# Performance work log

Hardware: AMD Instinct MI355X
Metric: run time of the kernel (lower is better)

Reference implementation:

```python
import jax, jax.numpy as jnp
import numpy as np

N, E, L, HEADS, HID = 50000, 600000, 4, 8, 128
IN_C, OUT_C = 64, 64
D_HEAD = HID // HEADS


def _layer_norm(x, g, b, eps=1e-5):
    m = jnp.mean(x, axis=-1, keepdims=True)
    v = jnp.mean((x - m) ** 2, axis=-1, keepdims=True)
    return (x - m) * jax.lax.rsqrt(v + eps) * g + b


def _transformer_conv(h, src, dst, Wq, bq, Wk, bk, Wv, bv, Ws, bs, Wbeta):
    # PyG TransformerConv with beta=True, concat=True. src=edge_index[0] (j), dst=edge_index[1] (i).
    n, f = h.shape
    q = (h @ Wq.T + bq)[dst].reshape(-1, HEADS, D_HEAD)   # [E,H,D] query at destination
    k = (h @ Wk.T + bk)[src].reshape(-1, HEADS, D_HEAD)   # [E,H,D] key at source
    v = (h @ Wv.T + bv)[src].reshape(-1, HEADS, D_HEAD)   # [E,H,D] value at source
    alpha = jnp.sum(q * k, axis=-1) / float(np.sqrt(D_HEAD))  # [E,H]
    amax = jax.ops.segment_max(alpha, dst, num_segments=n)     # [N,H] segment softmax (stable)
    ex = jnp.exp(alpha - amax[dst])
    denom = jax.ops.segment_sum(ex, dst, num_segments=n)
    a = ex / (denom[dst] + 1e-16)                              # [E,H]
    out = jax.ops.segment_sum((a[:, :, None] * v).reshape(-1, f), dst, num_segments=n)  # [N,F]
    x_r = h @ Ws.T + bs                                        # root/skip transform
    beta = jax.nn.sigmoid(jnp.concatenate([out, x_r, out - x_r], axis=-1) @ Wbeta.T)    # [N,1]
    return beta * x_r + (1.0 - beta) * out


def _forward(x, src, dst, Wi, bi, Wq, bq, Wk, bk, Wv, bv, Ws, bs, Wbeta, ln_g, ln_b, W1, b1, W2, b2, Wo, bo):
    h = jax.nn.gelu(x @ Wi.T + bi, approximate=False)
    for i in range(L):
        res = h
        h = _transformer_conv(h, src, dst, Wq[i], bq[i], Wk[i], bk[i], Wv[i], bv[i], Ws[i], bs[i], Wbeta[i])
        h = _layer_norm(h + res, ln_g[i], ln_b[i])
        res = h
        f = jax.nn.gelu(h @ W1[i].T + b1[i], approximate=False) @ W2[i].T + b2[i]
        h = f + res
    return h @ Wo.T + bo


def setup_inputs() -> dict:
    key = jax.random.key(0)
    ks = jax.random.split(key, 24)
    rn = lambda k, shp, s=0.05: (jax.random.normal(k, shp, jnp.float32) * s)
    x = jax.random.normal(ks[0], (N, IN_C), jnp.float32)
    edge_index = jax.random.randint(ks[1], (2, E), 0, N, dtype=jnp.int64)
    return {
        "x": x,
        "edge_index": edge_index,
        "Wi": rn(ks[2], (HID, IN_C)), "bi": jnp.zeros((HID,), jnp.float32),
        "Wq": rn(ks[3], (L, HID, HID)), "bq": jnp.zeros((L, HID), jnp.float32),
        "Wk": rn(ks[4], (L, HID, HID)), "bk": jnp.zeros((L, HID), jnp.float32),
        "Wv": rn(ks[5], (L, HID, HID)), "bv": jnp.zeros((L, HID), jnp.float32),
        "Ws": rn(ks[6], (L, HID, HID)), "bs": jnp.zeros((L, HID), jnp.float32),
        "Wbeta": rn(ks[7], (L, 1, 3 * HID)),
        "ln_g": jnp.ones((L, HID), jnp.float32), "ln_b": jnp.zeros((L, HID), jnp.float32),
        "W1": rn(ks[8], (L, 4 * HID, HID)), "b1": jnp.zeros((L, 4 * HID), jnp.float32),
        "W2": rn(ks[9], (L, HID, 4 * HID)), "b2": jnp.zeros((L, HID), jnp.float32),
        "Wo": rn(ks[10], (OUT_C, HID)), "bo": jnp.zeros((OUT_C,), jnp.float32),
    }


def reference(x, edge_index, Wi, bi, Wq, bq, Wk, bk, Wv, bv, Ws, bs, Wbeta, ln_g, ln_b, W1, b1, W2, b2, Wo, bo):
    src, dst = edge_index[0], edge_index[1]
    return _forward(x, src, dst, Wi, bi, Wq, bq, Wk, bk, Wv, bv, Ws, bs, Wbeta, ln_g, ln_b, W1, b1, W2, b2, Wo, bo)
```

## Files before the change

### kernel.cpp

```cpp
#include <hip/hip_runtime.h>
#include <cmath>

#define HIDC   128
#define LAYERS 4
#define IN_C   64
#define OUT_C  64

typedef _Float16 h16x8 __attribute__((ext_vector_type(8)));
typedef _Float16 h16x2 __attribute__((ext_vector_type(2)));
typedef float    f32x4 __attribute__((ext_vector_type(4)));

__device__ __forceinline__ float gelu_f(float x) {
    return 0.5f * x * (1.0f + erff(x * 0.70710678118654752f));
}

__device__ __forceinline__ void cvt8(const float4& a, const float4& b, h16x8& h) {
    h[0]=(_Float16)a.x; h[1]=(_Float16)a.y; h[2]=(_Float16)a.z; h[3]=(_Float16)a.w;
    h[4]=(_Float16)b.x; h[5]=(_Float16)b.y; h[6]=(_Float16)b.z; h[7]=(_Float16)b.w;
}
__device__ __forceinline__ void load16(const float* p, _Float16* d) {
    float4 v0 = *(const float4*)p,     v1 = *(const float4*)(p + 4);
    float4 v2 = *(const float4*)(p+8), v3 = *(const float4*)(p + 12);
    h16x8 h0, h1; cvt8(v0, v1, h0); cvt8(v2, v3, h1);
    *(h16x8*)d = h0; *(h16x8*)(d + 8) = h1;
}
__device__ __forceinline__ void load16(const _Float16* p, _Float16* d) {
    *(h16x8*)d = *(const h16x8*)p; *(h16x8*)(d + 8) = *(const h16x8*)(p + 8);
}
__device__ __forceinline__ void zero16(_Float16* d) {
    h16x8 z = {};
    *(h16x8*)d = z; *(h16x8*)(d + 8) = z;
}

__global__ void count_deg_k(const int* __restrict__ dst, int* __restrict__ cnt, int E) {
    int i = blockIdx.x * blockDim.x + threadIdx.x;
    if (i < E) atomicAdd(&cnt[dst[i]], 1);
}

__global__ __launch_bounds__(1024)
void scan_k(const int* __restrict__ cnt, int* __restrict__ rowptr, int n) {
    __shared__ int partials[1024];
    int tid = threadIdx.x;
    int per = (n + 1023) / 1024;
    int start = tid * per;
    int end = start + per; if (end > n) end = n;
    int s = 0;
    for (int i = start; i < end; ++i) s += cnt[i];
    partials[tid] = s;
    __syncthreads();
    for (int off = 1; off < 1024; off <<= 1) {
        int v = (tid >= off) ? partials[tid - off] : 0;
        __syncthreads();
        partials[tid] += v;
        __syncthreads();
    }
    int run = (tid == 0) ? 0 : partials[tid - 1];
    for (int i = start; i < end; ++i) { rowptr[i] = run; run += cnt[i]; }
    if (tid == 1023) rowptr[n] = partials[1023];
}

__global__ void scatter_k(const int* __restrict__ src, const int* __restrict__ dst,
                          const int* __restrict__ rowptr, int* __restrict__ cnt,
                          int* __restrict__ csrc, int E) {
    int i = blockIdx.x * blockDim.x + threadIdx.x;
    if (i < E) {
        int d = dst[i];
        int pos = rowptr[d] + atomicAdd(&cnt[d], 1);
        csrc[pos] = src[i];
    }
}

template<int ACT, bool RES, bool NGUARD, typename AT, typename CT>
__device__ __forceinline__ void gemm_core(
    const AT* __restrict__ A, const float* __restrict__ Wt,
    const float* __restrict__ bias, const float* __restrict__ resid,
    CT* __restrict__ Ct, int M, int K, int ncs, int colbase, int nclim)
{
    __shared__ __align__(16) _Float16 As[128 * 40];
    __shared__ __align__(16) _Float16 Bs[128 * 40];
    const int tid  = threadIdx.x;
    const int lane = tid & 63;
    const int wave = tid >> 6;
    const int wr = wave >> 1, wc = wave & 1;
    const int row0 = blockIdx.y * 128;

    f32x4 acc[4][4] = {};

    const int srow = tid >> 1;
    const int skc  = (tid & 1) * 16;
    const int fr   = lane & 15;
    const int fk   = (lane >> 4) * 8;

    for (int k0 = 0; k0 < K; k0 += 32) {
        {
            int gr = row0 + srow;
            _Float16* d = As + srow * 40 + skc;
            if (gr < M) load16(A + (size_t)gr * K + k0 + skc, d);
            else        zero16(d);
        }
        {
            int gc = colbase + srow;
            _Float16* d = Bs + srow * 40 + skc;
            if (!NGUARD || gc < nclim) load16(Wt + (size_t)gc * K + k0 + skc, d);
            else                       zero16(d);
        }
        __syncthreads();
        h16x8 af[4], bf[4];
#pragma unroll
        for (int mi = 0; mi < 4; ++mi)
            af[mi] = *(const h16x8*)(As + (wr * 64 + mi * 16 + fr) * 40 + fk);
#pragma unroll
        for (int ni = 0; ni < 4; ++ni)
            bf[ni] = *(const h16x8*)(Bs + (wc * 64 + ni * 16 + fr) * 40 + fk);
#pragma unroll
        for (int mi = 0; mi < 4; ++mi)
#pragma unroll
            for (int ni = 0; ni < 4; ++ni)
                acc[mi][ni] = __builtin_amdgcn_mfma_f32_16x16x32_f16(af[mi], bf[ni], acc[mi][ni], 0, 0, 0);
        __syncthreads();
    }

    const int rbase = row0 + wr * 64 + ((lane >> 4) * 4);
    const int cbase = colbase + wc * 64 + fr;
#pragma unroll
    for (int mi = 0; mi < 4; ++mi) {
#pragma unroll
        for (int j = 0; j < 4; ++j) {
            int r = rbase + mi * 16 + j;
            if (r >= M) continue;
            size_t rb = (size_t)r * ncs;
#pragma unroll
            for (int ni = 0; ni < 4; ++ni) {
                int c = cbase + ni * 16;
                if (NGUARD && c >= nclim) continue;
                float v = acc[mi][ni][j] + bias[c];
                if (ACT == 1) v = gelu_f(v);
                if (RES) v += resid[rb + c];
                Ct[rb + c] = (CT)v;
            }
        }
    }
}

template<int ACT, bool RES, bool NGUARD, typename AT, typename CT>
__global__ __launch_bounds__(256)
void gemm_f16_k(const AT* __restrict__ A, const float* __restrict__ W,
                const float* __restrict__ bias, const float* __restrict__ resid,
                CT* __restrict__ C, int M, int NC, int K) {
    gemm_core<ACT, RES, NGUARD, AT, CT>(A, W, bias, resid, C, M, K, NC, blockIdx.x * 128, NC);
}

__global__ __launch_bounds__(256)
void qkvs_k(const float* __restrict__ A,
            const float* __restrict__ Wq, const float* __restrict__ Wk,
            const float* __restrict__ Wv, const float* __restrict__ Wvs,
            const float* __restrict__ bq, const float* __restrict__ bk,
            const float* __restrict__ bv, const float* __restrict__ bs,
            _Float16* __restrict__ qh, _Float16* __restrict__ kv,
            float* __restrict__ sb, int M) {
    __shared__ __align__(16) _Float16 As[128 * 136];
    __shared__ __align__(16) _Float16 Bs[128 * 136];
    const int tid  = threadIdx.x;
    const int lane = tid & 63;
    const int wave = tid >> 6;
    const int wr = wave >> 1, wc = wave & 1;
    const int row0 = blockIdx.x * 128;
    const int srow  = tid >> 1;
    const int shalf = (tid & 1) * 64;
    const int fr = lane & 15;

    {
        int gr = row0 + srow;
        _Float16* d = As + srow * 136 + shalf;
        if (gr < M) {
            const float* p = A + (size_t)gr * 128 + shalf;
#pragma unroll
            for (int u = 0; u < 4; ++u) load16(p + u * 16, d + u * 16);
        } else {
#pragma unroll
            for (int u = 0; u < 4; ++u) zero16(d + u * 16);
        }
    }

    for (int w = 0; w < 4; ++w) {
        const float* Wp = (w == 0) ? Wq : (w == 1) ? Wk : (w == 2) ? Wv : Wvs;
        const float* bp = (w == 0) ? bq : (w == 1) ? bk : (w == 2) ? bv : bs;
        {
            const float* p = Wp + (size_t)srow * 128 + shalf;
            _Float16* d = Bs + srow * 136 + shalf;
#pragma unroll
            for (int u = 0; u < 4; ++u) load16(p + u * 16, d + u * 16);
        }
        __syncthreads();
        f32x4 acc[4][4] = {};
#pragma unroll
        for (int ks = 0; ks < 4; ++ks) {
            const int fk = ks * 32 + (lane >> 4) * 8;
            h16x8 af[4], bf[4];
#pragma unroll
            for (int mi = 0; mi < 4; ++mi)
                af[mi] = *(const h16x8*)(As + (wr * 64 + mi * 16 + fr) * 136 + fk);
#pragma unroll
            for (int ni = 0; ni < 4; ++ni)
                bf[ni] = *(const h16x8*)(Bs + (wc * 64 + ni * 16 + fr) * 136 + fk);
#pragma unroll
            for (int mi = 0; mi < 4; ++mi)
#pragma unroll
                for (int ni = 0; ni < 4; ++ni)
                    acc[mi][ni] = __builtin_amdgcn_mfma_f32_16x16x32_f16(af[mi], bf[ni], acc[mi][ni], 0, 0, 0);
        }
        __syncthreads();

        const int rbase = row0 + wr * 64 + ((lane >> 4) * 4);
        const int cbase = wc * 64 + fr;
#pragma unroll
        for (int mi = 0; mi < 4; ++mi) {
#pragma unroll
            for (int j = 0; j < 4; ++j) {
                int r = rbase + mi * 16 + j;
                if (r >= M) continue;
#pragma unroll
                for (int ni = 0; ni < 4; ++ni) {
                    int c = cbase + ni * 16;
                    float v = acc[mi][ni][j] + bp[c];
                    if (w == 0)      qh[(size_t)r * 128 + c] = (_Float16)v;
                    else if (w == 1) kv[(size_t)r * 256 + c] = (_Float16)v;
                    else if (w == 2) kv[(size_t)r * 256 + 128 + c] = (_Float16)v;
                    else             sb[(size_t)r * 128 + c] = v;
                }
            }
        }
    }
}

__global__ __launch_bounds__(256)
void attn_ln_k(const _Float16* __restrict__ qh, const _Float16* __restrict__ kv,
               const int* __restrict__ rowptr, const int* __restrict__ csrc,
               const float* __restrict__ xr, const float* __restrict__ res,
               const float* __restrict__ Wb, const float* __restrict__ g_,
               const float* __restrict__ b_, float* __restrict__ out, int n) {
    int node = (int)((blockIdx.x * (size_t)blockDim.x + threadIdx.x) >> 6);
    int lane = threadIdx.x & 63;
    if (node >= n) return;
    const int g = lane & 7;
    const int h = lane >> 3;

    const _Float16* qp = qh + (size_t)node * 128 + h * 16;
    h16x8 q0 = *(const h16x8*)(qp);
    h16x8 q1 = *(const h16x8*)(qp + 8);

    float ssum = 0.f;
    float acc[16] = {};
    const int e0 = rowptr[node], e1 = rowptr[node + 1];
    for (int eb = e0; eb < e1; eb += 8) {
        int e = eb + g;
        bool val = (e < e1);
        int s = csrc[val ? e : (e1 - 1)];
        const _Float16* kp = kv + (size_t)s * 256 + h * 16;
        h16x8 k0 = *(const h16x8*)(kp);
        h16x8 k1 = *(const h16x8*)(kp + 8);
        h16x8 v0 = *(const h16x8*)(kp + 128);
        h16x8 v1 = *(const h16x8*)(kp + 136);
        float d = 0.f;
#pragma unroll
        for (int j = 0; j < 8; ++j) d += (float)k0[j] * (float)q0[j];
#pragma unroll
        for (int j = 0; j < 8; ++j) d += (float)k1[j] * (float)q1[j];
        float w = val ? __expf(d * 0.25f) : 0.f;
        ssum += w;
#pragma unroll
        for (int j = 0; j < 8; ++j) acc[j]     += w * (float)v0[j];
#pragma unroll
        for (int j = 0; j < 8; ++j) acc[8 + j] += w * (float)v1[j];
    }
#pragma unroll
    for (int m = 1; m < 8; m <<= 1) {
        ssum += __shfl_xor(ssum, m);
#pragma unroll
        for (int j = 0; j < 16; ++j) acc[j] += __shfl_xor(acc[j], m);
    }
    float inv = 1.f / (ssum + 1e-16f);
    const bool s0b = g & 1, s1b = g & 2, s2b = g & 4;
    float t0 = s0b ? acc[2]  : acc[0],  t1 = s0b ? acc[6]  : acc[4];
    float t2 = s0b ? acc[10] : acc[8],  t3 = s0b ? acc[14] : acc[12];
    float u0 = s1b ? t1 : t0,           u1 = s1b ? t3 : t2;
    float ox = (s2b ? u1 : u0) * inv;
    float p0 = s0b ? acc[3]  : acc[1],  p1 = s0b ? acc[7]  : acc[5];
    float p2 = s0b ? acc[11] : acc[9],  p3 = s0b ? acc[15] : acc[13];
    float w0 = s1b ? p1 : p0,           w1 = s1b ? p3 : p2;
    float oy = (s2b ? w1 : w0) * inv;

    size_t base = (size_t)node * HIDC + lane * 2;
    int c = lane * 2;
    float2 r  = *(const float2*)(xr + base);
    float2 wb0 = *(const float2*)(Wb + c);
    float2 wb1 = *(const float2*)(Wb + HIDC + c);
    float2 wb2 = *(const float2*)(Wb + 2 * HIDC + c);
    float part = ox * wb0.x + oy * wb0.y
               + r.x * wb1.x + r.y * wb1.y
               + (ox - r.x) * wb2.x + (oy - r.y) * wb2.y;
#pragma unroll
    for (int mk = 1; mk < 64; mk <<= 1) part += __shfl_xor(part, mk);
    float beta = 1.f / (1.f + __expf(-part));
    float2 rs = *(const float2*)(res + base);
    float tx = beta * r.x + (1.f - beta) * ox + rs.x;
    float ty = beta * r.y + (1.f - beta) * oy + rs.y;
    float sum = tx + ty;
#pragma unroll
    for (int mk = 1; mk < 64; mk <<= 1) sum += __shfl_xor(sum, mk);
    float mean = sum * (1.f / 128.f);
    float dx = tx - mean, dy = ty - mean;
    float vs = dx * dx + dy * dy;
#pragma unroll
    for (int mk = 1; mk < 64; mk <<= 1) vs += __shfl_xor(vs, mk);
    float rstd = 1.f / sqrtf(vs * (1.f / 128.f) + 1e-5f);
    float2 gg = *(const float2*)(g_ + c);
    float2 bb = *(const float2*)(b_ + c);
    float2 oo = make_float2(dx * rstd * gg.x + bb.x, dy * rstd * gg.y + bb.y);
    *(float2*)(out + base) = oo;
}

extern "C" void kernel_launch(void* const* d_in, const int* in_sizes, int n_in,
                              void* d_out, int out_size, void* d_ws, size_t ws_size,
                              hipStream_t stream) {
    const float* x    = (const float*)d_in[0];
    const int*   ei   = (const int*)d_in[1];
    const float* Wi   = (const float*)d_in[2];
    const float* bi   = (const float*)d_in[3];
    const float* Wq   = (const float*)d_in[4];
    const float* bq   = (const float*)d_in[5];
    const float* Wk   = (const float*)d_in[6];
    const float* bk   = (const float*)d_in[7];
    const float* Wv   = (const float*)d_in[8];
    const float* bv   = (const float*)d_in[9];
    const float* Ws_  = (const float*)d_in[10];
    const float* bs   = (const float*)d_in[11];
    const float* Wbeta= (const float*)d_in[12];
    const float* ln_g = (const float*)d_in[13];
    const float* ln_b = (const float*)d_in[14];
    const float* W1   = (const float*)d_in[15];
    const float* b1   = (const float*)d_in[16];
    const float* W2   = (const float*)d_in[17];
    const float* b2   = (const float*)d_in[18];
    const float* Wo   = (const float*)d_in[19];
    const float* bo   = (const float*)d_in[20];
    float* outp = (float*)d_out;

    const int Nn = in_sizes[0] / IN_C;
    const int Ee = in_sizes[1] / 2;
    const int* srcI = ei;
    const int* dstI = ei + Ee;

    float* ws = (float*)d_ws;
    size_t n128 = (size_t)Nn * HIDC;
    float*     h   = ws;
    float*     h2  = h  + n128;
    _Float16*  qh  = (_Float16*)(h2 + n128);
    _Float16*  kv  = qh + (size_t)Nn * 128;
    float*     sb  = (float*)(kv + (size_t)Nn * 256);
    _Float16*  ffn = qh;
    int* rowptr = (int*)(sb + n128);
    int* cnt    = rowptr + (Nn + 1);
    int* csrc   = cnt + Nn;

    hipMemsetAsync(cnt, 0, Nn * sizeof(int), stream);
    count_deg_k<<<(Ee + 255) / 256, 256, 0, stream>>>(dstI, cnt, Ee);
    scan_k<<<1, 1024, 0, stream>>>(cnt, rowptr, Nn);
    hipMemsetAsync(cnt, 0, Nn * sizeof(int), stream);
    scatter_k<<<(Ee + 255) / 256, 256, 0, stream>>>(srcI, dstI, rowptr, cnt, csrc, Ee);

    const int mblk = (Nn + 127) / 128;
    dim3 blk(256);

    gemm_f16_k<1, false, false, float, float><<<dim3(1, mblk), blk, 0, stream>>>(x, Wi, bi, nullptr, h, Nn, HIDC, IN_C);

    int nwaveblk = (Nn + 3) / 4;

    for (int l = 0; l < LAYERS; ++l) {
        const float* Wq_l = Wq + (size_t)l * HIDC * HIDC;
        const float* Wk_l = Wk + (size_t)l * HIDC * HIDC;
        const float* Wv_l = Wv + (size_t)l * HIDC * HIDC;
        const float* Ws_l = Ws_ + (size_t)l * HIDC * HIDC;
        const float* bq_l = bq + (size_t)l * HIDC;
        const float* bk_l = bk + (size_t)l * HIDC;
        const float* bv_l = bv + (size_t)l * HIDC;
        const float* bs_l = bs + (size_t)l * HIDC;
        const float* Wb_l = Wbeta + (size_t)l * 3 * HIDC;
        const float* g_l  = ln_g + (size_t)l * HIDC;
        const float* b_l  = ln_b + (size_t)l * HIDC;
        const float* W1_l = W1 + (size_t)l * 4 * HIDC * HIDC;
        const float* b1_l = b1 + (size_t)l * 4 * HIDC;
        const float* W2_l = W2 + (size_t)l * HIDC * 4 * HIDC;
        const float* b2_l = b2 + (size_t)l * HIDC;

        qkvs_k<<<dim3(mblk), blk, 0, stream>>>(h, Wq_l, Wk_l, Wv_l, Ws_l,
                                               bq_l, bk_l, bv_l, bs_l,
                                               qh, kv, sb, Nn);

        attn_ln_k<<<nwaveblk, blk, 0, stream>>>(qh, kv, rowptr, csrc,
                                                sb, h, Wb_l, g_l, b_l, h2, Nn);

        gemm_f16_k<1, false, false, float, _Float16><<<dim3(4, mblk), blk, 0, stream>>>(h2, W1_l, b1_l, nullptr, ffn, Nn, 4 * HIDC, HIDC);
        gemm_f16_k<0, true, false, _Float16, float><<<dim3(1, mblk), blk, 0, stream>>>(ffn, W2_l, b2_l, h2, h, Nn, HIDC, 4 * HIDC);
    }

    gemm_f16_k<0, false, true, float, float><<<dim3(1, mblk), blk, 0, stream>>>(h, Wo, bo, nullptr, outp, Nn, OUT_C, HIDC);
}
```

Measured before the change: 1.038 ms.

## Parallelize CSR row-pointer scan and reuse staged activations across FFN1 column tiles

Replaces the single-block 1024-thread prefix scan with a three-kernel multi-block scan (per-block scan, block-sum scan, offset add), removing a serial bottleneck in CSR construction. Also adds a dedicated FFN first-layer kernel that loads each 128-row activation tile into shared memory once and loops over the four 128-column weight chunks, instead of launching four column blocks that each re-read and re-convert the activation tile. This trades grid-level parallelism for the FFN1 GEMM (fewer blocks, serial over output chunks) for reduced global reads and conversions, and adds two extra kernel launches for the scan.

```diff
diff --git a/kernel.cpp b/kernel.cpp
--- a/kernel.cpp
+++ b/kernel.cpp
@@ -37,26 +37,55 @@
     if (i < E) atomicAdd(&cnt[dst[i]], 1);
 }
 
-__global__ __launch_bounds__(1024)
-void scan_k(const int* __restrict__ cnt, int* __restrict__ rowptr, int n) {
-    __shared__ int partials[1024];
-    int tid = threadIdx.x;
-    int per = (n + 1023) / 1024;
-    int start = tid * per;
-    int end = start + per; if (end > n) end = n;
-    int s = 0;
-    for (int i = start; i < end; ++i) s += cnt[i];
-    partials[tid] = s;
+__global__ __launch_bounds__(256)
+void scan1_k(const int* __restrict__ cnt, int* __restrict__ pref,
+             int* __restrict__ bsum, int n) {
+    __shared__ int part[256];
+    const int b = blockIdx.x, t = threadIdx.x;
+    const int i0 = b * 1024 + t * 4;
+    int v0 = (i0 + 0 < n) ? cnt[i0 + 0] : 0;
+    int v1 = (i0 + 1 < n) ? cnt[i0 + 1] : 0;
+    int v2 = (i0 + 2 < n) ? cnt[i0 + 2] : 0;
+    int v3 = (i0 + 3 < n) ? cnt[i0 + 3] : 0;
+    int s = v0 + v1 + v2 + v3;
+    part[t] = s;
     __syncthreads();
-    for (int off = 1; off < 1024; off <<= 1) {
-        int v = (tid >= off) ? partials[tid - off] : 0;
-        __syncthreads();
-        partials[tid] += v;
-        __syncthreads();
-    }
-    int run = (tid == 0) ? 0 : partials[tid - 1];
-    for (int i = start; i < end; ++i) { rowptr[i] = run; run += cnt[i]; }
-    if (tid == 1023) rowptr[n] = partials[1023];
+    for (int off = 1; off < 256; off <<= 1) {
+        int x = (t >= off) ? part[t - off] : 0;
+        __syncthreads();
+        part[t] += x;
+        __syncthreads();
+    }
+    int excl = part[t] - s;
+    if (i0 + 0 < n) pref[i0 + 0] = excl;           excl += v0;
+    if (i0 + 1 < n) pref[i0 + 1] = excl;           excl += v1;
+    if (i0 + 2 < n) pref[i0 + 2] = excl;           excl += v2;
+    if (i0 + 3 < n) pref[i0 + 3] = excl;
+    if (t == 255) bsum[b] = part[255];
+}
+
+__global__ void scan2_k(const int* __restrict__ bsum, int* __restrict__ boff,
+                        int nb, int* __restrict__ rowptr_n) {
+    int lane = threadIdx.x;
+    int carry = 0;
+    for (int base = 0; base < nb; base += 64) {
+        int i = base + lane;
+        int v = (i < nb) ? bsum[i] : 0;
+        int incl = v;
+        for (int off = 1; off < 64; off <<= 1) {
+            int x = __shfl_up(incl, off);
+            if (lane >= off) incl += x;
+        }
+        if (i < nb) boff[i] = carry + incl - v;
+        carry += __shfl(incl, 63);
+    }
+    if (lane == 0) *rowptr_n = carry;
+}
+
+__global__ __launch_bounds__(256)
+void scan3_k(int* __restrict__ pref, const int* __restrict__ boff, int n) {
+    int i = blockIdx.x * blockDim.x + threadIdx.x;
+    if (i < n) pref[i] += boff[i >> 10];
 }
 
 __global__ void scatter_k(const int* __restrict__ src, const int* __restrict__ dst,
@@ -227,6 +256,80 @@
                     else if (w == 1) kv[(size_t)r * 256 + c] = (_Float16)v;
                     else if (w == 2) kv[(size_t)r * 256 + 128 + c] = (_Float16)v;
                     else             sb[(size_t)r * 128 + c] = v;
+                }
+            }
+        }
+    }
+}
+
+__global__ __launch_bounds__(256)
+void ffn1_k(const float* __restrict__ A, const float* __restrict__ W1,
+            const float* __restrict__ b1, _Float16* __restrict__ ffn, int M) {
+    __shared__ __align__(16) _Float16 As[128 * 136];
+    __shared__ __align__(16) _Float16 Bs[128 * 136];
+    const int tid  = threadIdx.x;
+    const int lane = tid & 63;
+    const int wave = tid >> 6;
+    const int wr = wave >> 1, wc = wave & 1;
+    const int row0 = blockIdx.x * 128;
+    const int srow  = tid >> 1;
+    const int shalf = (tid & 1) * 64;
+    const int fr = lane & 15;
+
+    {
+        int gr = row0 + srow;
+        _Float16* d = As + srow * 136 + shalf;
+        if (gr < M) {
+            const float* p = A + (size_t)gr * 128 + shalf;
+#pragma unroll
+            for (int u = 0; u < 4; ++u) load16(p + u * 16, d + u * 16);
+        } else {
+#pragma unroll
+            for (int u = 0; u < 4; ++u) zero16(d + u * 16);
+        }
+    }
+
+    for (int w = 0; w < 4; ++w) {
+        const float* Wp = W1 + (size_t)w * 128 * 128;
+        {
+            const float* p = Wp + (size_t)srow * 128 + shalf;
+            _Float16* d = Bs + srow * 136 + shalf;
+#pragma unroll
+            for (int u = 0; u < 4; ++u) load16(p + u * 16, d + u * 16);
+        }
+        __syncthreads();
+        f32x4 acc[4][4] = {};
+#pragma unroll
+        for (int ks = 0; ks < 4; ++ks) {
+            const int fk = ks * 32 + (lane >> 4) * 8;
+            h16x8 af[4], bf[4];
+#pragma unroll
+            for (int mi = 0; mi < 4; ++mi)
+                af[mi] = *(const h16x8*)(As + (wr * 64 + mi * 16 + fr) * 136 + fk);
+#pragma unroll
+            for (int ni = 0; ni < 4; ++ni)
+                bf[ni] = *(const h16x8*)(Bs + (wc * 64 + ni * 16 + fr) * 136 + fk);
+#pragma unroll
+            for (int mi = 0; mi < 4; ++mi)
+#pragma unroll
+                for (int ni = 0; ni < 4; ++ni)
+                    acc[mi][ni] = __builtin_amdgcn_mfma_f32_16x16x32_f16(af[mi], bf[ni], acc[mi][ni], 0, 0, 0);
+        }
+        __syncthreads();
+
+        const int rbase = row0 + wr * 64 + ((lane >> 4) * 4);
+        const int cbase = wc * 64 + fr;
+#pragma unroll
+        for (int mi = 0; mi < 4; ++mi) {
+#pragma unroll
+            for (int j = 0; j < 4; ++j) {
+                int r = rbase + mi * 16 + j;
+                if (r >= M) continue;
+#pragma unroll
+                for (int ni = 0; ni < 4; ++ni) {
+                    int c = cbase + ni * 16;
+                    float v = acc[mi][ni][j] + b1[w * 128 + c];
+                    ffn[(size_t)r * 512 + w * 128 + c] = (_Float16)gelu_f(v);
                 }
             }
         }
@@ -362,10 +465,16 @@
     int* rowptr = (int*)(sb + n128);
     int* cnt    = rowptr + (Nn + 1);
     int* csrc   = cnt + Nn;
+    int* bsum   = csrc + Ee;
+    int* boff   = bsum + 1024;
+
+    const int nb = (Nn + 1023) / 1024;
 
     hipMemsetAsync(cnt, 0, Nn * sizeof(int), stream);
     count_deg_k<<<(Ee + 255) / 256, 256, 0, stream>>>(dstI, cnt, Ee);
-    scan_k<<<1, 1024, 0, stream>>>(cnt, rowptr, Nn);
+    scan1_k<<<nb, 256, 0, stream>>>(cnt, rowptr, bsum, Nn);
+    scan2_k<<<1, 64, 0, stream>>>(bsum, boff, nb, rowptr + Nn);
+    scan3_k<<<(Nn + 255) / 256, 256, 0, stream>>>(rowptr, boff, Nn);
     hipMemsetAsync(cnt, 0, Nn * sizeof(int), stream);
     scatter_k<<<(Ee + 255) / 256, 256, 0, stream>>>(srcI, dstI, rowptr, cnt, csrc, Ee);
 
@@ -400,7 +509,7 @@
         attn_ln_k<<<nwaveblk, blk, 0, stream>>>(qh, kv, rowptr, csrc,
                                                 sb, h, Wb_l, g_l, b_l, h2, Nn);
 
-        gemm_f16_k<1, false, false, float, _Float16><<<dim3(4, mblk), blk, 0, stream>>>(h2, W1_l, b1_l, nullptr, ffn, Nn, 4 * HIDC, HIDC);
+        ffn1_k<<<dim3(mblk), blk, 0, stream>>>(h2, W1_l, b1_l, ffn, Nn);
         gemm_f16_k<0, true, false, _Float16, float><<<dim3(1, mblk), blk, 0, stream>>>(ffn, W2_l, b2_l, h2, h, Nn, HIDC, 4 * HIDC);
     }
 
```

New measurement: 1.059 ms. No clear change (+2.0%).

## Parallelize CSR prefix scan and split QKVS projection across blocks

Applied to the files above, without the earlier changes.

Replaces the single-block 1024-thread serial-chunk scan with a three-kernel hierarchical scan (block-local scan, single-wave scan of block sums, add-back), removing a latency-bound serial stage. The fused QKVS kernel now uses one block per (projection, row tile) with K-tiled 32-wide shared staging, which quadruples the grid and shrinks shared memory for higher occupancy. The trade-off is that the activation tile is reloaded four times from global memory, and two extra small launches are added for the scan.

```diff
diff --git a/kernel.cpp b/kernel.cpp
--- a/kernel.cpp
+++ b/kernel.cpp
@@ -7,7 +7,6 @@
 #define OUT_C  64
 
 typedef _Float16 h16x8 __attribute__((ext_vector_type(8)));
-typedef _Float16 h16x2 __attribute__((ext_vector_type(2)));
 typedef float    f32x4 __attribute__((ext_vector_type(4)));
 
 __device__ __forceinline__ float gelu_f(float x) {
@@ -37,26 +36,55 @@
     if (i < E) atomicAdd(&cnt[dst[i]], 1);
 }
 
-__global__ __launch_bounds__(1024)
-void scan_k(const int* __restrict__ cnt, int* __restrict__ rowptr, int n) {
-    __shared__ int partials[1024];
-    int tid = threadIdx.x;
-    int per = (n + 1023) / 1024;
-    int start = tid * per;
-    int end = start + per; if (end > n) end = n;
-    int s = 0;
-    for (int i = start; i < end; ++i) s += cnt[i];
-    partials[tid] = s;
+__global__ __launch_bounds__(256)
+void scan1_k(const int* __restrict__ cnt, int* __restrict__ pref,
+             int* __restrict__ bsum, int n) {
+    __shared__ int part[256];
+    const int b = blockIdx.x, t = threadIdx.x;
+    const int i0 = b * 1024 + t * 4;
+    int v0 = (i0 + 0 < n) ? cnt[i0 + 0] : 0;
+    int v1 = (i0 + 1 < n) ? cnt[i0 + 1] : 0;
+    int v2 = (i0 + 2 < n) ? cnt[i0 + 2] : 0;
+    int v3 = (i0 + 3 < n) ? cnt[i0 + 3] : 0;
+    int s = v0 + v1 + v2 + v3;
+    part[t] = s;
     __syncthreads();
-    for (int off = 1; off < 1024; off <<= 1) {
-        int v = (tid >= off) ? partials[tid - off] : 0;
-        __syncthreads();
-        partials[tid] += v;
-        __syncthreads();
-    }
-    int run = (tid == 0) ? 0 : partials[tid - 1];
-    for (int i = start; i < end; ++i) { rowptr[i] = run; run += cnt[i]; }
-    if (tid == 1023) rowptr[n] = partials[1023];
+    for (int off = 1; off < 256; off <<= 1) {
+        int x = (t >= off) ? part[t - off] : 0;
+        __syncthreads();
+        part[t] += x;
+        __syncthreads();
+    }
+    int excl = part[t] - s;
+    if (i0 + 0 < n) pref[i0 + 0] = excl;           excl += v0;
+    if (i0 + 1 < n) pref[i0 + 1] = excl;           excl += v1;
+    if (i0 + 2 < n) pref[i0 + 2] = excl;           excl += v2;
+    if (i0 + 3 < n) pref[i0 + 3] = excl;
+    if (t == 255) bsum[b] = part[255];
+}
+
+__global__ void scan2_k(const int* __restrict__ bsum, int* __restrict__ boff,
+                        int nb, int* __restrict__ rowptr_n) {
+    int lane = threadIdx.x;
+    int carry = 0;
+    for (int base = 0; base < nb; base += 64) {
+        int i = base + lane;
+        int v = (i < nb) ? bsum[i] : 0;
+        int incl = v;
+        for (int off = 1; off < 64; off <<= 1) {
+            int x = __shfl_up(incl, off);
+            if (lane >= off) incl += x;
+        }
+        if (i < nb) boff[i] = carry + incl - v;
+        carry += __shfl(incl, 63);
+    }
+    if (lane == 0) *rowptr_n = carry;
+}
+
+__global__ __launch_bounds__(256)
+void scan3_k(int* __restrict__ pref, const int* __restrict__ boff, int n) {
+    int i = blockIdx.x * blockDim.x + threadIdx.x;
+    if (i < n) pref[i] += boff[i >> 10];
 }
 
 __global__ void scatter_k(const int* __restrict__ src, const int* __restrict__ dst,
@@ -158,76 +186,68 @@
             const float* __restrict__ bv, const float* __restrict__ bs,
             _Float16* __restrict__ qh, _Float16* __restrict__ kv,
             float* __restrict__ sb, int M) {
-    __shared__ __align__(16) _Float16 As[128 * 136];
-    __shared__ __align__(16) _Float16 Bs[128 * 136];
+    __shared__ __align__(16) _Float16 As[128 * 40];
+    __shared__ __align__(16) _Float16 Bs[128 * 40];
+    const int proj = blockIdx.x;
+    const float* Wt = (proj == 0) ? Wq : (proj == 1) ? Wk : (proj == 2) ? Wv : Wvs;
+    const float* bp = (proj == 0) ? bq : (proj == 1) ? bk : (proj == 2) ? bv : bs;
+
     const int tid  = threadIdx.x;
     const int lane = tid & 63;
     const int wave = tid >> 6;
     const int wr = wave >> 1, wc = wave & 1;
-    const int row0 = blockIdx.x * 128;
-    const int srow  = tid >> 1;
-    const int shalf = (tid & 1) * 64;
-    const int fr = lane & 15;
-
-    {
-        int gr = row0 + srow;
-        _Float16* d = As + srow * 136 + shalf;
-        if (gr < M) {
-            const float* p = A + (size_t)gr * 128 + shalf;
-#pragma unroll
-            for (int u = 0; u < 4; ++u) load16(p + u * 16, d + u * 16);
-        } else {
-#pragma unroll
-            for (int u = 0; u < 4; ++u) zero16(d + u * 16);
-        }
-    }
-
-    for (int w = 0; w < 4; ++w) {
-        const float* Wp = (w == 0) ? Wq : (w == 1) ? Wk : (w == 2) ? Wv : Wvs;
-        const float* bp = (w == 0) ? bq : (w == 1) ? bk : (w == 2) ? bv : bs;
+    const int row0 = blockIdx.y * 128;
+
+    f32x4 acc[4][4] = {};
+
+    const int srow = tid >> 1;
+    const int skc  = (tid & 1) * 16;
+    const int fr   = lane & 15;
+    const int fk   = (lane >> 4) * 8;
+
+    for (int k0 = 0; k0 < 128; k0 += 32) {
         {
-            const float* p = Wp + (size_t)srow * 128 + shalf;
-            _Float16* d = Bs + srow * 136 + shalf;
-#pragma unroll
-            for (int u = 0; u < 4; ++u) load16(p + u * 16, d + u * 16);
-        }
-        __syncthreads();
-        f32x4 acc[4][4] = {};
-#pragma unroll
-        for (int ks = 0; ks < 4; ++ks) {
-            const int fk = ks * 32 + (lane >> 4) * 8;
-            h16x8 af[4], bf[4];
-#pragma unroll
-            for (int mi = 0; mi < 4; ++mi)
-                af[mi] = *(const h16x8*)(As + (wr * 64 + mi * 16 + fr) * 136 + fk);
+            int gr = row0 + srow;
+            _Float16* d = As + srow * 40 + skc;
+            if (gr < M) load16(A + (size_t)gr * 128 + k0 + skc, d);
+            else        zero16(d);
+        }
+        {
+            _Float16* d = Bs + srow * 40 + skc;
+            load16(Wt + (size_t)srow * 128 + k0 + skc, d);
+        }
+        __syncthreads();
+        h16x8 af[4], bf[4];
+#pragma unroll
+        for (int mi = 0; mi < 4; ++mi)
+            af[mi] = *(const h16x8*)(As + (wr * 64 + mi * 16 + fr) * 40 + fk);
+#pragma unroll
+        for (int ni = 0; ni < 4; ++ni)
+            bf[ni] = *(const h16x8*)(Bs + (wc * 64 + ni * 16 + fr) * 40 + fk);
+#pragma unroll
+        for (int mi = 0; mi < 4; ++mi)
 #pragma unroll
             for (int ni = 0; ni < 4; ++ni)
-                bf[ni] = *(const h16x8*)(Bs + (wc * 64 + ni * 16 + fr) * 136 + fk);
-#pragma unroll
-            for (int mi = 0; mi < 4; ++mi)
-#pragma unroll
-                for (int ni = 0; ni < 4; ++ni)
-                    acc[mi][ni] = __builtin_amdgcn_mfma_f32_16x16x32_f16(af[mi], bf[ni], acc[mi][ni], 0, 0, 0);
-        }
-        __syncthreads();
-
-        const int rbase = row0 + wr * 64 + ((lane >> 4) * 4);
-        const int cbase = wc * 64 + fr;
-#pragma unroll
-        for (int mi = 0; mi < 4; ++mi) {
-#pragma unroll
-            for (int j = 0; j < 4; ++j) {
-                int r = rbase + mi * 16 + j;
-                if (r >= M) continue;
-#pragma unroll
-                for (int ni = 0; ni < 4; ++ni) {
-                    int c = cbase + ni * 16;
-                    float v = acc[mi][ni][j] + bp[c];
-                    if (w == 0)      qh[(size_t)r * 128 + c] = (_Float16)v;
-                    else if (w == 1) kv[(size_t)r * 256 + c] = (_Float16)v;
-                    else if (w == 2) kv[(size_t)r * 256 + 128 + c] = (_Float16)v;
-                    else             sb[(size_t)r * 128 + c] = v;
-                }
+                acc[mi][ni] = __builtin_amdgcn_mfma_f32_16x16x32_f16(af[mi], bf[ni], acc[mi][ni], 0, 0, 0);
+        __syncthreads();
+    }
+
+    const int rbase = row0 + wr * 64 + ((lane >> 4) * 4);
+    const int cbase = wc * 64 + fr;
+#pragma unroll
+    for (int mi = 0; mi < 4; ++mi) {
+#pragma unroll
+        for (int j = 0; j < 4; ++j) {
+            int r = rbase + mi * 16 + j;
+            if (r >= M) continue;
+#pragma unroll
+            for (int ni = 0; ni < 4; ++ni) {
+                int c = cbase + ni * 16;
+                float v = acc[mi][ni][j] + bp[c];
+                if (proj == 0)      qh[(size_t)r * 128 + c] = (_Float16)v;
+                else if (proj == 1) kv[(size_t)r * 256 + c] = (_Float16)v;
+                else if (proj == 2) kv[(size_t)r * 256 + 128 + c] = (_Float16)v;
+                else                sb[(size_t)r * 128 + c] = v;
             }
         }
     }
@@ -362,10 +382,16 @@
     int* rowptr = (int*)(sb + n128);
     int* cnt    = rowptr + (Nn + 1);
     int* csrc   = cnt + Nn;
+    int* bsum   = csrc + Ee;
+    int* boff   = bsum + 1024;
+
+    const int nb = (Nn + 1023) / 1024;
 
     hipMemsetAsync(cnt, 0, Nn * sizeof(int), stream);
     count_deg_k<<<(Ee + 255) / 256, 256, 0, stream>>>(dstI, cnt, Ee);
-    scan_k<<<1, 1024, 0, stream>>>(cnt, rowptr, Nn);
+    scan1_k<<<nb, 256, 0, stream>>>(cnt, rowptr, bsum, Nn);
+    scan2_k<<<1, 64, 0, stream>>>(bsum, boff, nb, rowptr + Nn);
+    scan3_k<<<(Nn + 255) / 256, 256, 0, stream>>>(rowptr, boff, Nn);
     hipMemsetAsync(cnt, 0, Nn * sizeof(int), stream);
     scatter_k<<<(Ee + 255) / 256, 256, 0, stream>>>(srcI, dstI, rowptr, cnt, csrc, Ee);
 
@@ -393,9 +419,9 @@
         const float* W2_l = W2 + (size_t)l * HIDC * 4 * HIDC;
         const float* b2_l = b2 + (size_t)l * HIDC;
 
-        qkvs_k<<<dim3(mblk), blk, 0, stream>>>(h, Wq_l, Wk_l, Wv_l, Ws_l,
-                                               bq_l, bk_l, bv_l, bs_l,
-                                               qh, kv, sb, Nn);
+        qkvs_k<<<dim3(4, mblk), blk, 0, stream>>>(h, Wq_l, Wk_l, Wv_l, Ws_l,
+                                                  bq_l, bk_l, bv_l, bs_l,
+                                                  qh, kv, sb, Nn);
 
         attn_ln_k<<<nwaveblk, blk, 0, stream>>>(qh, kv, rowptr, csrc,
                                                 sb, h, Wb_l, g_l, b_l, h2, Nn);
```

Result: slower. 1.076 ms (+3.6%).
